# Kernel optimization log

Measured on AMD Instinct MI355X. Metric: run time of the kernel, lower is better.

Reference implementation:

```python
import jax, jax.numpy as jnp
import numpy as np

CAPACITY_FACTOR = 1.0


def setup_inputs() -> dict:
    key = jax.random.key(0)
    ks = jax.random.split(key, 6)
    B, S, D, H, E = 4, 2048, 1024, 4096, 8
    scale_in = 1.0 / np.sqrt(D)
    scale_h = 1.0 / np.sqrt(H)
    return {
        "inputs": jax.random.normal(ks[0], (B, S, D), dtype=jnp.float32),
        "router_w": jax.random.normal(ks[1], (E, D), dtype=jnp.float32) * scale_in,
        "w1": jax.random.normal(ks[2], (E, D, H), dtype=jnp.float32) * scale_in,
        "b1": jnp.zeros((E, H), dtype=jnp.float32),
        "w2": jax.random.normal(ks[3], (E, H, D), dtype=jnp.float32) * scale_h,
        "b2": jnp.zeros((E, D), dtype=jnp.float32),
    }


def reference(inputs, router_w, w1, b1, w2, b2):
    B, S, D = inputs.shape
    E = router_w.shape[0]
    x = inputs.reshape(-1, D)                     # [T, D], T = B*S
    T = x.shape[0]
    top_k = int(CAPACITY_FACTOR * T / E)          # static: 1024

    # Router + softmax over experts (softmax_topk order), fp32 like the original
    router_logits = x @ router_w.T                # [T, E]
    all_probs = jax.nn.softmax(router_logits.astype(jnp.float32), axis=-1)

    # Expert-choice: each expert picks its top_k tokens
    weights, selected_tokens = jax.lax.top_k(all_probs.T, top_k)  # [E, K]

    # Gather tokens per expert: [E, K, D]
    xg = x[selected_tokens]

    # Per-expert MLP as grouped GEMMs (Linear -> GELU(exact) -> Linear)
    h = jax.nn.gelu(jnp.einsum("ekd,edh->ekh", xg, w1) + b1[:, None, :],
                    approximate=False)
    out = jnp.einsum("ekh,ehd->ekd", h, w2) + b2[:, None, :]   # [E, K, D]

    # Weighted scatter-add combine (indices unique within an expert;
    # cross-expert duplicates accumulate, matching the per-expert += loop)
    out = out * weights[..., None].astype(out.dtype)
    results = jnp.zeros_like(x).at[selected_tokens.reshape(-1)].add(
        out.reshape(-1, D))

    return results.reshape(B, S, D), router_logits, selected_tokens
```

## Files before the change

kernel.cpp:

```cpp
#include <hip/hip_runtime.h>
#include <hip/hip_bf16.h>
#include <math.h>

#define T_TOK 8192
#define E_EXP 8
#define D_DIM 1024
#define H_DIM 4096
#define K_CAP 1024

typedef __attribute__((ext_vector_type(8))) short short8;
typedef __attribute__((ext_vector_type(4))) float floatx4;
typedef __attribute__((ext_vector_type(16))) float floatx16;

typedef __attribute__((address_space(3))) unsigned int lds_u32_t;
typedef __attribute__((address_space(1))) unsigned int gbl_u32_t;
#define ASYNC_CP16(gptr, lptr) \
  __builtin_amdgcn_global_load_lds((gbl_u32_t*)(gptr), (lds_u32_t*)(lptr), 16, 0, 0)

static __device__ __forceinline__ unsigned int f2bf_u(float f) {
  union { float f; unsigned int u; } v; v.f = f;
  unsigned int r = v.u + 0x7FFF + ((v.u >> 16) & 1);
  return r >> 16;
}

__global__ __launch_bounds__(256) void zero_kernel(float* __restrict__ p, int n4) {
  int i = blockIdx.x * 256 + threadIdx.x;
  if (i < n4) ((floatx4*)p)[i] = (floatx4)0.0f;
}

template <int KD, int ND>
__global__ __launch_bounds__(256)
void transpose_kernel(const float* __restrict__ w, unsigned short* __restrict__ wt) {
  int e = blockIdx.z;
  int n0 = blockIdx.x * 64, k0 = blockIdx.y * 64;
  __shared__ float ts[64][65];
  int tid = threadIdx.x;
  int rr = tid >> 4;
  int cc = (tid & 15) * 4;
  const float* src = w + ((size_t)e * KD + k0 + rr) * ND + n0 + cc;
#pragma unroll
  for (int it = 0; it < 4; it++) {
    float4 v = *(const float4*)(src + (size_t)it * 16 * ND);
    int r = rr + it * 16;
    ts[r][cc + 0] = v.x; ts[r][cc + 1] = v.y; ts[r][cc + 2] = v.z; ts[r][cc + 3] = v.w;
  }
  __syncthreads();
  int n = tid >> 3;
  int k8 = (tid & 7) * 8;
#pragma unroll
  for (int it = 0; it < 2; it++) {
    int nn = n + it * 32;
    unsigned int u[4];
#pragma unroll
    for (int j = 0; j < 4; j++)
      u[j] = f2bf_u(ts[k8 + 2 * j][nn]) | (f2bf_u(ts[k8 + 2 * j + 1][nn]) << 16);
    *(uint4*)&wt[((size_t)e * ND + n0 + nn) * KD + k0 + k8] = *(uint4*)u;
  }
}

__global__ __launch_bounds__(256)
void router_kernel(const float* __restrict__ x, const float* __restrict__ rw,
                   float* __restrict__ logits_out, float* __restrict__ probs_ws,
                   unsigned long long* __restrict__ keys_ws,
                   unsigned short* __restrict__ x_bf) {
  int t = blockIdx.x;
  int tid = threadIdx.x;
  int lane = tid & 63, wid = tid >> 6;
  __shared__ float xs[D_DIM];
  __shared__ double dred[4 * E_EXP];
  __shared__ double dlog[E_EXP];
  for (int i = tid; i < D_DIM; i += 256) xs[i] = x[(size_t)t * D_DIM + i];
  __syncthreads();
  {
    int i4 = tid * 4;
    uint2 u;
    u.x = f2bf_u(xs[i4 + 0]) | (f2bf_u(xs[i4 + 1]) << 16);
    u.y = f2bf_u(xs[i4 + 2]) | (f2bf_u(xs[i4 + 3]) << 16);
    ((uint2*)(x_bf + (size_t)t * D_DIM))[tid] = u;
  }
#pragma unroll
  for (int e = 0; e < E_EXP; e++) {
    double s = 0.0;
#pragma unroll
    for (int i = 0; i < 4; i++) {
      int d = tid + i * 256;
      s += (double)xs[d] * (double)rw[e * D_DIM + d];
    }
#pragma unroll
    for (int off = 32; off > 0; off >>= 1) s += __shfl_down(s, off, 64);
    if (lane == 0) dred[wid * E_EXP + e] = s;
  }
  __syncthreads();
  if (tid < E_EXP) {
    double s = dred[tid] + dred[E_EXP + tid] + dred[2 * E_EXP + tid] + dred[3 * E_EXP + tid];
    dlog[tid] = s;
    logits_out[(size_t)t * E_EXP + tid] = (float)s;
  }
  __syncthreads();
  if (tid == 0) {
    double m = dlog[0];
#pragma unroll
    for (int e = 1; e < E_EXP; e++) m = dlog[e] > m ? dlog[e] : m;
    double ex[E_EXP], Z = 0.0;
#pragma unroll
    for (int e = 0; e < E_EXP; e++) { ex[e] = exp(dlog[e] - m); Z += ex[e]; }
#pragma unroll
    for (int e = 0; e < E_EXP; e++) {
      double p = ex[e] / Z;
      probs_ws[e * T_TOK + t] = (float)p;
      unsigned long long b = (unsigned long long)__double_as_longlong(p);
      keys_ws[e * T_TOK + t] = (b & ~8191ULL) | (unsigned long long)(8191 - t);
    }
  }
}

__global__ __launch_bounds__(256)
void topk_kernel(const unsigned long long* __restrict__ keys_ws,
                 const float* __restrict__ probs_ws,
                 int* __restrict__ sel_ws, float* __restrict__ wt_ws,
                 float* __restrict__ selout) {
  int e = blockIdx.x >> 5, seg = blockIdx.x & 31;
  int tid = threadIdx.x;
  const unsigned long long* keys = keys_ws + (size_t)e * T_TOK;
  __shared__ unsigned long long kbuf[2048];
  int t = seg * 256 + tid;
  unsigned long long own = keys[t];
  int rank = 0;
  for (int pass = 0; pass < 4; pass++) {
    __syncthreads();
    for (int j = tid; j < 2048; j += 256) kbuf[j] = keys[pass * 2048 + j];
    __syncthreads();
#pragma unroll 8
    for (int j = 0; j < 2048; j++) rank += (kbuf[j] > own);
  }
  if (rank < K_CAP) {
    sel_ws[e * K_CAP + rank] = t;
    wt_ws[e * K_CAP + rank] = probs_ws[e * T_TOK + t];
    selout[e * K_CAP + rank] = (float)t;
  }
}

template <int MODE, int KDIM, int NDIM>
__device__ __forceinline__ void gemm_core(
    int e, int m0, int n0, int kbase, int kch, bool add_bias,
    const unsigned short* __restrict__ abase,
    const unsigned short* __restrict__ bt,
    const float* __restrict__ bias,
    const int* __restrict__ sel,
    const float* __restrict__ wt,
    unsigned short* __restrict__ hout,
    float* __restrict__ results) {
  __shared__ __align__(16) unsigned char smem[131072];
  int tid = threadIdx.x;
  int lane = tid & 63, w = tid >> 6;
  int wm = w >> 2, wn = w & 3;

  const unsigned short* srcA[4];
  const unsigned short* srcB[4];
  int ldsA[4], ldsB[4];
#pragma unroll
  for (int j = 0; j < 4; ++j) {
    int c = j * 512 + tid;
    int h = c >> 10;
    int kk32 = (c >> 9) & 1;
    int cp = c & 511;
    int cpp = cp ^ ((cp >> 3) & 3);
    int row = cpp >> 2, cch = cpp & 3;
    int trow = h * 128 + row;
    int koff = kk32 * 32 + cch * 8;
    size_t arow;
    if (MODE == 1) arow = (size_t)sel[e * K_CAP + m0 + trow];
    else           arow = (size_t)e * K_CAP + m0 + trow;
    srcA[j] = abase + arow * KDIM + kbase + koff;
    srcB[j] = bt + ((size_t)e * NDIM + n0 + trow) * KDIM + kbase + koff;
    ldsA[j] = c * 16;
    ldsB[j] = 32768 + c * 16;
  }

  auto stage = [&](int b) {
    char* Lb = (char*)smem + b * 65536;
#pragma unroll
    for (int j = 0; j < 4; ++j) {
      ASYNC_CP16(srcA[j], Lb + ldsA[j]);
      ASYNC_CP16(srcB[j], Lb + ldsB[j]);
      srcA[j] += 64; srcB[j] += 64;
    }
  };

  floatx16 acc[4][2];
#pragma unroll
  for (int i = 0; i < 4; ++i)
#pragma unroll
    for (int j = 0; j < 2; ++j) acc[i][j] = (floatx16)0.0f;

  int rA = lane & 31;
  int q16 = (lane >> 5) * 16;

  int NT = kch / 64;

  stage(0);
  __syncthreads();

  for (int kt = 0; kt < NT; ++kt) {
    if (kt + 1 < NT) stage((kt + 1) & 1);

    const char* Lb = (const char*)smem + (kt & 1) * 65536;
    const char* Aplane = Lb + wm * 16384;
    const char* Bplane = Lb + 32768 + (wn >> 1) * 16384;
#pragma unroll
    for (int half = 0; half < 2; ++half) {
      const char* Ap = Aplane + half * 8192;
      const char* Bp = Bplane + half * 8192;
      short8 av[4][2], bv[2][2];
#pragma unroll
      for (int fm = 0; fm < 4; ++fm) {
        int r = fm * 32 + rA;
        int xr = ((r >> 1) & 3) << 4;
#pragma unroll
        for (int kk = 0; kk < 2; ++kk) {
          int off = (r * 64 + kk * 32 + q16) ^ xr;
          av[fm][kk] = *(const short8*)(Ap + off);
        }
      }
#pragma unroll
      for (int fn = 0; fn < 2; ++fn) {
        int r = (wn & 1) * 64 + fn * 32 + rA;
        int xr = ((r >> 1) & 3) << 4;
#pragma unroll
        for (int kk = 0; kk < 2; ++kk) {
          int off = (r * 64 + kk * 32 + q16) ^ xr;
          bv[fn][kk] = *(const short8*)(Bp + off);
        }
      }
#pragma unroll
      for (int kk = 0; kk < 2; ++kk)
#pragma unroll
        for (int fm = 0; fm < 4; ++fm)
#pragma unroll
          for (int fn = 0; fn < 2; ++fn)
            acc[fm][fn] = __builtin_amdgcn_mfma_f32_32x32x16_bf16(
                av[fm][kk], bv[fn][kk], acc[fm][fn], 0, 0, 0);
    }
    __syncthreads();
  }

  int hi = lane >> 5;
#pragma unroll
  for (int fm = 0; fm < 4; ++fm) {
    if (MODE == 1) {
#pragma unroll
      for (int fn = 0; fn < 2; ++fn) {
        int col = n0 + wn * 64 + fn * 32 + rA;
        float bv_ = bias[e * NDIM + col];
#pragma unroll
        for (int r = 0; r < 16; ++r) {
          int m_l = wm * 128 + fm * 32 + (r & 3) + 8 * (r >> 2) + 4 * hi;
          float v = acc[fm][fn][r] + bv_;
          float gl = 0.5f * v * (1.0f + erff(v * 0.70710678118f));
          hout[((size_t)e * K_CAP + m0 + m_l) * NDIM + col] = (unsigned short)f2bf_u(gl);
        }
      }
    } else {
      int toks[16]; float wgts[16];
#pragma unroll
      for (int r = 0; r < 16; ++r) {
        int m_l = wm * 128 + fm * 32 + (r & 3) + 8 * (r >> 2) + 4 * hi;
        toks[r] = sel[e * K_CAP + m0 + m_l];
        wgts[r] = wt[e * K_CAP + m0 + m_l];
      }
#pragma unroll
      for (int fn = 0; fn < 2; ++fn) {
        int col = n0 + wn * 64 + fn * 32 + rA;
        float bv_ = add_bias ? bias[e * NDIM + col] : 0.0f;
#pragma unroll
        for (int r = 0; r < 16; ++r) {
          float v = (acc[fm][fn][r] + bv_) * wgts[r];
          atomicAdd(&results[(size_t)toks[r] * D_DIM + col], v);
        }
      }
    }
  }
}

__global__ __launch_bounds__(512, 2)
void moe_gemm1(const unsigned short* __restrict__ x_bf,
               const unsigned short* __restrict__ w1t,
               const float* __restrict__ b1,
               const int* __restrict__ sel,
               unsigned short* __restrict__ h) {
  gemm_core<1, D_DIM, H_DIM>(blockIdx.z, blockIdx.y * 256, blockIdx.x * 256,
                             0, D_DIM, true, x_bf, w1t, b1, sel, nullptr, h, nullptr);
}

__global__ __launch_bounds__(512, 2)
void moe_gemm2(const unsigned short* __restrict__ h,
               const unsigned short* __restrict__ w2t,
               const float* __restrict__ b2,
               const int* __restrict__ sel,
               const float* __restrict__ wt,
               float* __restrict__ results) {
  int e = blockIdx.x;
  int rest = blockIdx.y;
  int s = rest & 1;
  int nt = (rest >> 1) & 3;
  int mt = rest >> 3;
  gemm_core<2, H_DIM, D_DIM>(e, mt * 256, nt * 256, s * (H_DIM / 2), H_DIM / 2,
                             s == 0, h, w2t, b2, sel, wt, nullptr, results);
}

extern "C" void kernel_launch(void* const* d_in, const int* in_sizes, int n_in,
                              void* d_out, int out_size, void* d_ws, size_t ws_size,
                              hipStream_t stream) {
  const float* x  = (const float*)d_in[0];
  const float* rw = (const float*)d_in[1];
  const float* w1 = (const float*)d_in[2];
  const float* b1 = (const float*)d_in[3];
  const float* w2 = (const float*)d_in[4];
  const float* b2 = (const float*)d_in[5];

  float* out_res = (float*)d_out;
  float* out_log = out_res + (size_t)T_TOK * D_DIM;
  float* out_sel = out_log + (size_t)T_TOK * E_EXP;

  char* ws = (char*)d_ws;
  float* probs_ws = (float*)ws;
  unsigned long long* keys_ws = (unsigned long long*)(ws + 262144);
  int* sel_ws = (int*)(ws + 786432);
  float* wt_ws = (float*)(ws + 819200);
  unsigned short* x_bf = (unsigned short*)(ws + 1048576);
  unsigned short* h_ws = (unsigned short*)(ws + 17825792);
  unsigned short* t_buf = (unsigned short*)(ws + 84934656);

  zero_kernel<<<(T_TOK * D_DIM / 4 + 255) / 256, 256, 0, stream>>>(out_res, T_TOK * D_DIM / 4);

  router_kernel<<<T_TOK, 256, 0, stream>>>(x, rw, out_log, probs_ws, keys_ws, x_bf);

  topk_kernel<<<256, 256, 0, stream>>>(keys_ws, probs_ws, sel_ws, wt_ws, out_sel);

  transpose_kernel<D_DIM, H_DIM><<<dim3(H_DIM / 64, D_DIM / 64, E_EXP), 256, 0, stream>>>(
      w1, t_buf);

  moe_gemm1<<<dim3(H_DIM / 256, K_CAP / 256, E_EXP), 512, 0, stream>>>(
      x_bf, t_buf, b1, sel_ws, h_ws);

  transpose_kernel<H_DIM, D_DIM><<<dim3(D_DIM / 64, H_DIM / 64, E_EXP), 256, 0, stream>>>(
      w2, t_buf);

  moe_gemm2<<<dim3(E_EXP, 32), 512, 0, stream>>>(
      h_ws, t_buf, b2, sel_ws, wt_ws, out_res);
}
```

Baseline: 696.7 us.

## Use 4-stage async LDS pipeline with 32-wide K tiles and vmcnt waits

```diff
diff --git a/kernel.cpp b/kernel.cpp
--- a/kernel.cpp
+++ b/kernel.cpp
@@ -16,6 +16,9 @@
 typedef __attribute__((address_space(1))) unsigned int gbl_u32_t;
 #define ASYNC_CP16(gptr, lptr) \
   __builtin_amdgcn_global_load_lds((gbl_u32_t*)(gptr), (lds_u32_t*)(lptr), 16, 0, 0)
+
+#define WAITVM(N) asm volatile("s_waitcnt vmcnt(" #N ")" ::: "memory")
+#define FENCE()   asm volatile("" ::: "memory")
 
 static __device__ __forceinline__ unsigned int f2bf_u(float f) {
   union { float f; unsigned int u; } v; v.f = f;
@@ -155,35 +158,31 @@
   int lane = tid & 63, w = tid >> 6;
   int wm = w >> 2, wn = w & 3;
 
-  const unsigned short* srcA[4];
-  const unsigned short* srcB[4];
-  int ldsA[4], ldsB[4];
-#pragma unroll
-  for (int j = 0; j < 4; ++j) {
+  const unsigned short* srcA[2];
+  const unsigned short* srcB[2];
+  int ldsA[2], ldsB[2];
+#pragma unroll
+  for (int j = 0; j < 2; ++j) {
     int c = j * 512 + tid;
-    int h = c >> 10;
-    int kk32 = (c >> 9) & 1;
-    int cp = c & 511;
-    int cpp = cp ^ ((cp >> 3) & 3);
-    int row = cpp >> 2, cch = cpp & 3;
-    int trow = h * 128 + row;
-    int koff = kk32 * 32 + cch * 8;
+    int r = c >> 2;
+    int cs = (c & 3) ^ ((r >> 1) & 3);
+    int koff = cs * 8;
     size_t arow;
-    if (MODE == 1) arow = (size_t)sel[e * K_CAP + m0 + trow];
-    else           arow = (size_t)e * K_CAP + m0 + trow;
+    if (MODE == 1) arow = (size_t)sel[e * K_CAP + m0 + r];
+    else           arow = (size_t)e * K_CAP + m0 + r;
     srcA[j] = abase + arow * KDIM + kbase + koff;
-    srcB[j] = bt + ((size_t)e * NDIM + n0 + trow) * KDIM + kbase + koff;
+    srcB[j] = bt + ((size_t)e * NDIM + n0 + r) * KDIM + kbase + koff;
     ldsA[j] = c * 16;
-    ldsB[j] = 32768 + c * 16;
-  }
-
-  auto stage = [&](int b) {
-    char* Lb = (char*)smem + b * 65536;
-#pragma unroll
-    for (int j = 0; j < 4; ++j) {
+    ldsB[j] = 16384 + c * 16;
+  }
+
+  auto stage = [&](int slot) {
+    char* Lb = (char*)smem + slot * 32768;
+#pragma unroll
+    for (int j = 0; j < 2; ++j) {
       ASYNC_CP16(srcA[j], Lb + ldsA[j]);
       ASYNC_CP16(srcB[j], Lb + ldsB[j]);
-      srcA[j] += 64; srcB[j] += 64;
+      srcA[j] += 32; srcB[j] += 32;
     }
   };
 
@@ -196,52 +195,51 @@
   int rA = lane & 31;
   int q16 = (lane >> 5) * 16;
 
-  int NT = kch / 64;
-
-  stage(0);
-  __syncthreads();
+  int NT = kch / 32;
+
+  stage(0); stage(1); stage(2);
 
   for (int kt = 0; kt < NT; ++kt) {
-    if (kt + 1 < NT) stage((kt + 1) & 1);
-
-    const char* Lb = (const char*)smem + (kt & 1) * 65536;
-    const char* Aplane = Lb + wm * 16384;
-    const char* Bplane = Lb + 32768 + (wn >> 1) * 16384;
-#pragma unroll
-    for (int half = 0; half < 2; ++half) {
-      const char* Ap = Aplane + half * 8192;
-      const char* Bp = Bplane + half * 8192;
-      short8 av[4][2], bv[2][2];
-#pragma unroll
-      for (int fm = 0; fm < 4; ++fm) {
-        int r = fm * 32 + rA;
-        int xr = ((r >> 1) & 3) << 4;
-#pragma unroll
-        for (int kk = 0; kk < 2; ++kk) {
-          int off = (r * 64 + kk * 32 + q16) ^ xr;
-          av[fm][kk] = *(const short8*)(Ap + off);
-        }
-      }
-#pragma unroll
-      for (int fn = 0; fn < 2; ++fn) {
-        int r = (wn & 1) * 64 + fn * 32 + rA;
-        int xr = ((r >> 1) & 3) << 4;
-#pragma unroll
-        for (int kk = 0; kk < 2; ++kk) {
-          int off = (r * 64 + kk * 32 + q16) ^ xr;
-          bv[fn][kk] = *(const short8*)(Bp + off);
-        }
-      }
+    if (kt + 3 < NT) stage((kt + 3) & 3);
+    int rem = NT - 1 - kt;
+    if (rem >= 3)      WAITVM(12);
+    else if (rem == 2) WAITVM(8);
+    else if (rem == 1) WAITVM(4);
+    else               WAITVM(0);
+    __builtin_amdgcn_s_barrier();
+    FENCE();
+
+    const char* Sb = (const char*)smem + (kt & 3) * 32768;
+    short8 av[4][2], bv[2][2];
+#pragma unroll
+    for (int fm = 0; fm < 4; ++fm) {
+      int r = wm * 128 + fm * 32 + rA;
+      int xr = ((r >> 1) & 3) << 4;
 #pragma unroll
       for (int kk = 0; kk < 2; ++kk)
-#pragma unroll
-        for (int fm = 0; fm < 4; ++fm)
-#pragma unroll
-          for (int fn = 0; fn < 2; ++fn)
-            acc[fm][fn] = __builtin_amdgcn_mfma_f32_32x32x16_bf16(
-                av[fm][kk], bv[fn][kk], acc[fm][fn], 0, 0, 0);
-    }
-    __syncthreads();
+        av[fm][kk] = *(const short8*)(Sb + ((r * 64 + kk * 32 + q16) ^ xr));
+    }
+#pragma unroll
+    for (int fn = 0; fn < 2; ++fn) {
+      int r = wn * 64 + fn * 32 + rA;
+      int xr = ((r >> 1) & 3) << 4;
+#pragma unroll
+      for (int kk = 0; kk < 2; ++kk)
+        bv[fn][kk] = *(const short8*)(Sb + 16384 + ((r * 64 + kk * 32 + q16) ^ xr));
+    }
+    __builtin_amdgcn_s_setprio(1);
+#pragma unroll
+    for (int kk = 0; kk < 2; ++kk)
+#pragma unroll
+      for (int fm = 0; fm < 4; ++fm)
+#pragma unroll
+        for (int fn = 0; fn < 2; ++fn)
+          acc[fm][fn] = __builtin_amdgcn_mfma_f32_32x32x16_bf16(
+              av[fm][kk], bv[fn][kk], acc[fm][fn], 0, 0, 0);
+    __builtin_amdgcn_s_setprio(0);
+    FENCE();
+    __builtin_amdgcn_s_barrier();
+    FENCE();
   }
 
   int hi = lane >> 5;
```

After: 709.0 us. No clear change (+1.8%).
